# Performance work log

Measured on AMD Instinct MI355X. Metric: run time of the kernel, lower is better.

The kernel has to match this reference:

```python
import jax, jax.numpy as jnp
import numpy as np

QMIN, QMAX = -128.0, 127.0  # int8 range

def setup_inputs() -> dict:
    key = jax.random.key(0)
    k1, k2 = jax.random.split(key)
    B, S, D_IN, D_OUT = 4, 2048, 4096, 4096
    x = jax.random.normal(k1, (B, S, D_IN), dtype=jnp.float32)
    # int8 weight stored as int32 (values in int8 range)
    weight = jax.random.randint(k2, (D_OUT, D_IN), -128, 128, dtype=jnp.int32)
    scale = jnp.array([0.02], dtype=jnp.float32)        # per-tensor weight scale
    input_scale = jnp.array([0.05], dtype=jnp.float32)  # static activation scale
    return {"x": x, "weight": weight, "scale": scale, "input_scale": input_scale}

def reference(x, weight, scale, input_scale):
    # quantize_static_quant_activations: round(x/input_scale) clamped to int8 range,
    # then direct_cast_dequantize back to fp32 (kept as fp32 here; values are integral).
    x_q = jnp.clip(jnp.round(x / input_scale), QMIN, QMAX)
    # direct_cast_dequantize(weight) -> fp32
    w = weight.astype(jnp.float32)
    # F.linear: x_q @ w.T  -> [B, S, D_OUT]
    out = jnp.einsum('bsi,oi->bso', x_q, w)
    # scale_dequantize with combined scale = input_scale * weight_scale
    return out * (input_scale * scale)
```

## Files before the change

kernel.cpp:

```cpp
#include <hip/hip_runtime.h>
#include <stdint.h>

typedef int v4i __attribute__((ext_vector_type(4)));

static constexpr int MDIM = 8192;
static constexpr int NDIM = 4096;
static constexpr int KDIM = 4096;
static constexpr int BM = 128;
static constexpr int BN = 128;
static constexpr int BK = 128;

static constexpr int QBLOCKS = (MDIM * KDIM / 16) / 256;
static constexpr int WBLOCKS = (NDIM * KDIM / 16) / 256;

__device__ __forceinline__ void lds_load16(const void* gptr, void* lptr) {
    __builtin_amdgcn_global_load_lds(
        (const __attribute__((address_space(1))) void*)(uintptr_t)gptr,
        (__attribute__((address_space(3))) void*)(uint32_t)(uintptr_t)lptr,
        16, 0, 0);
}

__device__ __forceinline__ int q1(float f, float s) {
    return (int)fminf(fmaxf(__builtin_rintf(f / s), -128.0f), 127.0f);
}
__device__ __forceinline__ int pack4(int a, int b, int c, int d) {
    return (a & 0xff) | ((b & 0xff) << 8) | ((c & 0xff) << 16) | ((d & 0xff) << 24);
}

__global__ __launch_bounds__(256) void prep_k(const float4* __restrict__ x,
                                              int4* __restrict__ xq,
                                              const int4* __restrict__ w,
                                              int4* __restrict__ wq,
                                              const float* __restrict__ s_in) {
    const int b = blockIdx.x;
    if (b < QBLOCKS) {
        const int i = b * 256 + threadIdx.x;
        const float s = s_in[0];
        const float4 v0 = x[4 * i + 0];
        const float4 v1 = x[4 * i + 1];
        const float4 v2 = x[4 * i + 2];
        const float4 v3 = x[4 * i + 3];
        int4 o;
        o.x = pack4(q1(v0.x, s), q1(v0.y, s), q1(v0.z, s), q1(v0.w, s));
        o.y = pack4(q1(v1.x, s), q1(v1.y, s), q1(v1.z, s), q1(v1.w, s));
        o.z = pack4(q1(v2.x, s), q1(v2.y, s), q1(v2.z, s), q1(v2.w, s));
        o.w = pack4(q1(v3.x, s), q1(v3.y, s), q1(v3.z, s), q1(v3.w, s));
        xq[i] = o;
    } else {
        const int i = (b - QBLOCKS) * 256 + threadIdx.x;
        const int4 a = w[4 * i + 0];
        const int4 c = w[4 * i + 1];
        const int4 d = w[4 * i + 2];
        const int4 e = w[4 * i + 3];
        int4 o;
        o.x = pack4(a.x, a.y, a.z, a.w);
        o.y = pack4(c.x, c.y, c.z, c.w);
        o.z = pack4(d.x, d.y, d.z, d.w);
        o.w = pack4(e.x, e.y, e.z, e.w);
        wq[i] = o;
    }
}

__global__ __launch_bounds__(256) void gemm_i8_k(const int8_t* __restrict__ A,
                                                 const int8_t* __restrict__ Bt,
                                                 float* __restrict__ C,
                                                 const float* __restrict__ w_scale,
                                                 const float* __restrict__ in_scale) {
    __shared__ int8_t sA[BM * BK];
    __shared__ int8_t sB[BN * BK];

    const int tid  = threadIdx.x;
    const int lane = tid & 63;
    const int wave = tid >> 6;
    const int bm = blockIdx.y;
    const int bn = blockIdx.x;

    const int wm = (wave >> 1) * 64;
    const int wn = (wave & 1) * 64;
    const int lm = lane & 15;
    const int q  = lane >> 4;

    v4i acc[4][4] = {};

    const int rr = wave * 32 + (lane >> 3);
    const int cc = ((lane & 7) ^ (lane >> 3)) * 16;
    const int8_t* gA0 = A  + (size_t)(bm * BM + rr) * KDIM + cc;
    const int8_t* gB0 = Bt + (size_t)(bn * BN + rr) * KDIM + cc;
    int8_t* lA0 = sA + wave * 4096;
    int8_t* lB0 = sB + wave * 4096;

    int aoff[2][4], boff[2][4];
#pragma unroll
    for (int ks = 0; ks < 2; ++ks)
#pragma unroll
        for (int t = 0; t < 4; ++t) {
            const int sw = (((ks * 4 + q) ^ (lm & 7)) << 4);
            aoff[ks][t] = (wm + t * 16 + lm) * BK + sw;
            boff[ks][t] = (wn + t * 16 + lm) * BK + sw;
        }

    for (int k0 = 0; k0 < KDIM; k0 += BK) {
        __syncthreads();
#pragma unroll
        for (int j = 0; j < 4; ++j) {
            lds_load16(gA0 + k0 + (size_t)j * (8 * KDIM), lA0 + j * 1024);
            lds_load16(gB0 + k0 + (size_t)j * (8 * KDIM), lB0 + j * 1024);
        }
        __syncthreads();

#pragma unroll
        for (int ks = 0; ks < 2; ++ks) {
            v4i av[4], bv[4];
#pragma unroll
            for (int t = 0; t < 4; ++t) {
                av[t] = *(const v4i*)(sA + aoff[ks][t]);
                bv[t] = *(const v4i*)(sB + boff[ks][t]);
            }
#pragma unroll
            for (int mt = 0; mt < 4; ++mt)
#pragma unroll
                for (int nt = 0; nt < 4; ++nt)
                    acc[mt][nt] = __builtin_amdgcn_mfma_i32_16x16x64_i8(
                        av[mt], bv[nt], acc[mt][nt], 0, 0, 0);
        }
    }

    const float fs = w_scale[0] * in_scale[0];
    const int crow = q * 4;
#pragma unroll
    for (int mt = 0; mt < 4; ++mt) {
#pragma unroll
        for (int nt = 0; nt < 4; ++nt) {
            const size_t n  = (size_t)bn * BN + wn + nt * 16 + lm;
            const size_t mb = (size_t)bm * BM + wm + mt * 16 + crow;
#pragma unroll
            for (int r = 0; r < 4; ++r) {
                C[(mb + r) * NDIM + n] = (float)acc[mt][nt][r] * fs;
            }
        }
    }
}

extern "C" void kernel_launch(void* const* d_in, const int* in_sizes, int n_in,
                              void* d_out, int out_size, void* d_ws, size_t ws_size,
                              hipStream_t stream) {
    const float* x        = (const float*)d_in[0];
    const int*   w        = (const int*)d_in[1];
    const float* w_scale  = (const float*)d_in[2];
    const float* in_scale = (const float*)d_in[3];
    float* out = (float*)d_out;

    int8_t* xq = (int8_t*)d_ws;
    int8_t* wq = xq + (size_t)MDIM * KDIM;

    prep_k<<<QBLOCKS + WBLOCKS, 256, 0, stream>>>(
        (const float4*)x, (int4*)xq, (const int4*)w, (int4*)wq, in_scale);

    dim3 grid(NDIM / BN, MDIM / BM);
    gemm_i8_k<<<grid, 256, 0, stream>>>(xq, wq, out, w_scale, in_scale);
}
```

Before: 398.8 us.

## Rewrite int8 GEMM as 256x256 tile with double-buffered LDS pipeline

```diff
diff --git a/kernel.cpp b/kernel.cpp
--- a/kernel.cpp
+++ b/kernel.cpp
@@ -6,9 +6,6 @@
 static constexpr int MDIM = 8192;
 static constexpr int NDIM = 4096;
 static constexpr int KDIM = 4096;
-static constexpr int BM = 128;
-static constexpr int BN = 128;
-static constexpr int BK = 128;
 
 static constexpr int QBLOCKS = (MDIM * KDIM / 16) / 256;
 static constexpr int WBLOCKS = (NDIM * KDIM / 16) / 256;
@@ -61,84 +58,120 @@
     }
 }
 
-__global__ __launch_bounds__(256) void gemm_i8_k(const int8_t* __restrict__ A,
-                                                 const int8_t* __restrict__ Bt,
-                                                 float* __restrict__ C,
-                                                 const float* __restrict__ w_scale,
-                                                 const float* __restrict__ in_scale) {
-    __shared__ int8_t sA[BM * BK];
-    __shared__ int8_t sB[BN * BK];
+__global__ __launch_bounds__(512, 2) void gemm_i8_k(const int8_t* __restrict__ A,
+                                                    const int8_t* __restrict__ Bt,
+                                                    float* __restrict__ C,
+                                                    const float* __restrict__ w_scale,
+                                                    const float* __restrict__ in_scale) {
+    __shared__ int8_t lds[131072];
 
     const int tid  = threadIdx.x;
     const int lane = tid & 63;
     const int wave = tid >> 6;
-    const int bm = blockIdx.y;
-    const int bn = blockIdx.x;
-
-    const int wm = (wave >> 1) * 64;
-    const int wn = (wave & 1) * 64;
+    const int wr = wave >> 2;
+    const int wc = wave & 3;
     const int lm = lane & 15;
     const int q  = lane >> 4;
 
-    v4i acc[4][4] = {};
+    const int bid = blockIdx.x;
+    const int xcd = bid & 7;
+    const int j   = bid >> 3;
+    const int bm  = (xcd >> 1) * 8 + (j >> 3);
+    const int bn  = (xcd & 1) * 8 + (j & 7);
 
-    const int rr = wave * 32 + (lane >> 3);
-    const int cc = ((lane & 7) ^ (lane >> 3)) * 16;
-    const int8_t* gA0 = A  + (size_t)(bm * BM + rr) * KDIM + cc;
-    const int8_t* gB0 = Bt + (size_t)(bn * BN + rr) * KDIM + cc;
-    int8_t* lA0 = sA + wave * 4096;
-    int8_t* lB0 = sB + wave * 4096;
+    const int srow  = tid >> 2;
+    const int sperm = ((tid & 3) ^ ((tid >> 3) & 3)) << 4;
+    const int8_t* gA = A  + (size_t)(bm * 256 + srow) * KDIM + sperm;
+    const int8_t* gB = Bt + (size_t)(bn * 256 + srow) * KDIM + sperm;
+    const int ldsT = tid * 16;
 
-    int aoff[2][4], boff[2][4];
-#pragma unroll
-    for (int ks = 0; ks < 2; ++ks)
-#pragma unroll
-        for (int t = 0; t < 4; ++t) {
-            const int sw = (((ks * 4 + q) ^ (lm & 7)) << 4);
-            aoff[ks][t] = (wm + t * 16 + lm) * BK + sw;
-            boff[ks][t] = (wn + t * 16 + lm) * BK + sw;
-        }
+#define STAGE(MATBASE, GSRC, slot, ks, kbyte)                                              \
+    lds_load16(GSRC + (kbyte) + (ks) * 64,                                                 \
+               lds + (MATBASE) + (slot) * 32768 + (ks) * 16384 + ldsT);                    \
+    lds_load16(GSRC + (kbyte) + (ks) * 64 + 524288,                                        \
+               lds + (MATBASE) + (slot) * 32768 + (ks) * 16384 + 8192 + ldsT);
 
-    for (int k0 = 0; k0 < KDIM; k0 += BK) {
-        __syncthreads();
-#pragma unroll
-        for (int j = 0; j < 4; ++j) {
-            lds_load16(gA0 + k0 + (size_t)j * (8 * KDIM), lA0 + j * 1024);
-            lds_load16(gB0 + k0 + (size_t)j * (8 * KDIM), lB0 + j * 1024);
-        }
-        __syncthreads();
+    const int fsw = ((q ^ ((lm >> 1) & 3)) << 4);
+    const int aB = (wr * 128 + lm) * 64 + fsw;
+    const int bB = 65536 + (wc * 64 + lm) * 64 + fsw;
 
-#pragma unroll
-        for (int ks = 0; ks < 2; ++ks) {
-            v4i av[4], bv[4];
-#pragma unroll
-            for (int t = 0; t < 4; ++t) {
-                av[t] = *(const v4i*)(sA + aoff[ks][t]);
-                bv[t] = *(const v4i*)(sB + boff[ks][t]);
-            }
-#pragma unroll
-            for (int mt = 0; mt < 4; ++mt)
-#pragma unroll
-                for (int nt = 0; nt < 4; ++nt)
-                    acc[mt][nt] = __builtin_amdgcn_mfma_i32_16x16x64_i8(
-                        av[mt], bv[nt], acc[mt][nt], 0, 0, 0);
-        }
+    v4i acc[8][4] = {{}};
+    v4i av[4], bv[4];
+
+#define RD(off) (*(const v4i*)(lds + (off)))
+
+#define PHASE(slot, ks, mh, STAGES, VMW)                                                   \
+    {                                                                                      \
+        if ((mh) == 0) {                                                                   \
+            bv[0] = RD(bB + (slot) * 32768 + (ks) * 16384 + 0 * 1024);                     \
+            bv[1] = RD(bB + (slot) * 32768 + (ks) * 16384 + 1 * 1024);                     \
+            bv[2] = RD(bB + (slot) * 32768 + (ks) * 16384 + 2 * 1024);                     \
+            bv[3] = RD(bB + (slot) * 32768 + (ks) * 16384 + 3 * 1024);                     \
+        }                                                                                  \
+        av[0] = RD(aB + (slot) * 32768 + (ks) * 16384 + (mh) * 4096 + 0 * 1024);           \
+        av[1] = RD(aB + (slot) * 32768 + (ks) * 16384 + (mh) * 4096 + 1 * 1024);           \
+        av[2] = RD(aB + (slot) * 32768 + (ks) * 16384 + (mh) * 4096 + 2 * 1024);           \
+        av[3] = RD(aB + (slot) * 32768 + (ks) * 16384 + (mh) * 4096 + 3 * 1024);           \
+        STAGES                                                                             \
+        __builtin_amdgcn_s_barrier();                                                      \
+        asm volatile("s_waitcnt lgkmcnt(0)" ::: "memory");                                 \
+        __builtin_amdgcn_s_setprio(1);                                                     \
+        _Pragma("unroll")                                                                  \
+        for (int mt = 0; mt < 4; ++mt)                                                     \
+            _Pragma("unroll")                                                              \
+            for (int nt = 0; nt < 4; ++nt)                                                 \
+                acc[(mh) * 4 + mt][nt] = __builtin_amdgcn_mfma_i32_16x16x64_i8(            \
+                    av[mt], bv[nt], acc[(mh) * 4 + mt][nt], 0, 0, 0);                      \
+        __builtin_amdgcn_s_setprio(0);                                                     \
+        VMW                                                                                \
+        __builtin_amdgcn_s_barrier();                                                      \
     }
 
+#define VM4 asm volatile("s_waitcnt vmcnt(4)" ::: "memory");
+#define VM0 asm volatile("s_waitcnt vmcnt(0)" ::: "memory");
+
+    STAGE(0, gA, 0, 0, 0) STAGE(65536, gB, 0, 0, 0)
+    STAGE(0, gA, 0, 1, 0) STAGE(65536, gB, 0, 1, 0)
+    STAGE(0, gA, 1, 0, 128) STAGE(65536, gB, 1, 0, 128)
+    VM4
+    __builtin_amdgcn_s_barrier();
+
+#pragma unroll 1
+    for (int i = 0; i < 15; ++i) {
+        const int kb = i * 256;
+        PHASE(0, 0, 0, STAGE(0, gA, 1, 1, kb + 128), )
+        PHASE(0, 0, 1, STAGE(65536, gB, 1, 1, kb + 128), )
+        PHASE(0, 1, 0, STAGE(0, gA, 0, 0, kb + 256), )
+        PHASE(0, 1, 1, STAGE(65536, gB, 0, 0, kb + 256), VM4)
+        PHASE(1, 0, 0, STAGE(0, gA, 0, 1, kb + 256), )
+        PHASE(1, 0, 1, STAGE(65536, gB, 0, 1, kb + 256), )
+        PHASE(1, 1, 0, STAGE(0, gA, 1, 0, kb + 384), )
+        PHASE(1, 1, 1, STAGE(65536, gB, 1, 0, kb + 384), VM4)
+    }
+    PHASE(0, 0, 0, STAGE(0, gA, 1, 1, 3968), )
+    PHASE(0, 0, 1, STAGE(65536, gB, 1, 1, 3968), )
+    PHASE(0, 1, 0, , )
+    PHASE(0, 1, 1, , VM0)
+    PHASE(1, 0, 0, , )
+    PHASE(1, 0, 1, , )
+    PHASE(1, 1, 0, , )
+    PHASE(1, 1, 1, , )
+
     const float fs = w_scale[0] * in_scale[0];
-    const int crow = q * 4;
+    float* Cb = C + (size_t)(bm * 256 + wr * 128 + q * 4) * NDIM + bn * 256 + wc * 64 + lm;
 #pragma unroll
-    for (int mt = 0; mt < 4; ++mt) {
+    for (int m = 0; m < 8; ++m)
 #pragma unroll
-        for (int nt = 0; nt < 4; ++nt) {
-            const size_t n  = (size_t)bn * BN + wn + nt * 16 + lm;
-            const size_t mb = (size_t)bm * BM + wm + mt * 16 + crow;
+        for (int n = 0; n < 4; ++n)
 #pragma unroll
-            for (int r = 0; r < 4; ++r) {
-                C[(mb + r) * NDIM + n] = (float)acc[mt][nt][r] * fs;
-            }
-        }
-    }
+            for (int r = 0; r < 4; ++r)
+                Cb[(size_t)(m * 16 + r) * NDIM + n * 16] = (float)acc[m][n][r] * fs;
+
+#undef STAGE
+#undef RD
+#undef PHASE
+#undef VM4
+#undef VM0
 }
 
 extern "C" void kernel_launch(void* const* d_in, const int* in_sizes, int n_in,
@@ -156,6 +189,5 @@
     prep_k<<<QBLOCKS + WBLOCKS, 256, 0, stream>>>(
         (const float4*)x, (int4*)xq, (const int4*)w, (int4*)wq, in_scale);
 
-    dim3 grid(NDIM / BN, MDIM / BM);
-    gemm_i8_k<<<grid, 256, 0, stream>>>(xq, wq, out, w_scale, in_scale);
+    gemm_i8_k<<<512, 512, 0, stream>>>(xq, wq, out, w_scale, in_scale);
 }
```

Measured after the change: 389.7 us. 1.02x faster.
